# Kernel optimization log

Hardware: AMD Instinct MI355X
Metric: run time of the kernel (lower is better)

Reference implementation:

```python
import jax, jax.numpy as jnp
import numpy as np

T, B, D = 512, 32, 1280

def setup_inputs() -> dict:
    key = jax.random.key(0)
    k1, k2, k3, k4 = jax.random.split(key, 4)
    # W_h ~ orthogonal*0.9 in the original; a small-scale gaussian keeps the
    # recurrence spectral radius < 1 so tanh stays in its active range.
    return {
        "x_seq": jax.random.normal(k1, (T, B, D), dtype=jnp.float32),
        "z_seq": jax.random.normal(k2, (T, B, D), dtype=jnp.float32),
        "h0": jnp.zeros((B, D), dtype=jnp.float32),
        "W_x": jax.random.normal(k3, (D, D), dtype=jnp.float32) * (1.0 / np.sqrt(D)),
        "W_h": jax.random.normal(k4, (D, D), dtype=jnp.float32) * (0.9 / np.sqrt(D)),
        "b": jnp.zeros((D,), dtype=jnp.float32),
    }

def reference(x_seq, z_seq, h0, W_x, W_h, b):
    # Gated Elman scan (Mamba-style output gate):
    #   h_t = tanh(W_x x_t + W_h h_{t-1} + b)
    #   y_t = h_t * silu(z_t)
    # Hoist the input projection into one big GEMM: [T,B,D] x [D,D]^T.
    x_proj = jnp.einsum('tbd,ed->tbe', x_seq, W_x) + b  # [T,B,D]
    Wh_T = W_h.T  # [D,D], h @ Wh_T == Linear(h)

    def step(h, inp):
        xp, z = inp
        h_new = jnp.tanh(xp + h @ Wh_T)          # [B,D]
        y = h_new * jax.nn.silu(z)               # gated output
        return h_new, y

    h_last, output = jax.lax.scan(step, h0, (x_proj, z_seq))
    return output, h_last
```

## Files before the change

### kernel.cpp

```cpp
#include <hip/hip_runtime.h>
#include <math.h>

#define TT 512
#define BB 32
#define DD 1280

__launch_bounds__(256) __global__
void xproj_gemm(const float* __restrict__ X, const float* __restrict__ Wx,
                const float* __restrict__ bias, float* __restrict__ XP)
{
    __shared__ __align__(16) float As[16][64];
    __shared__ __align__(16) float Bs[16][64];
    const int tid = threadIdx.x;
    const int n0 = blockIdx.x * 64;
    const int m0 = blockIdx.y * 64;
    const int lm = tid >> 2;
    const int lk = (tid & 3) << 2;
    const int tn = tid & 15;
    const int tm = tid >> 4;

    float acc[4][4] = {};
    for (int k0 = 0; k0 < DD; k0 += 16) {
        float4 av = *(const float4*)(X  + (size_t)(m0 + lm) * DD + k0 + lk);
        float4 bv = *(const float4*)(Wx + (size_t)(n0 + lm) * DD + k0 + lk);
        __syncthreads();
        As[lk + 0][lm] = av.x; As[lk + 1][lm] = av.y;
        As[lk + 2][lm] = av.z; As[lk + 3][lm] = av.w;
        Bs[lk + 0][lm] = bv.x; Bs[lk + 1][lm] = bv.y;
        Bs[lk + 2][lm] = bv.z; Bs[lk + 3][lm] = bv.w;
        __syncthreads();
#pragma unroll
        for (int k = 0; k < 16; ++k) {
            float4 a4 = *(const float4*)&As[k][tm << 2];
            float4 b4 = *(const float4*)&Bs[k][tn << 2];
            float a[4] = {a4.x, a4.y, a4.z, a4.w};
            float b[4] = {b4.x, b4.y, b4.z, b4.w};
#pragma unroll
            for (int i = 0; i < 4; ++i)
#pragma unroll
                for (int j = 0; j < 4; ++j)
                    acc[i][j] += a[i] * b[j];
        }
    }
    float4 bv = *(const float4*)(bias + n0 + (tn << 2));
    float bias4[4] = {bv.x, bv.y, bv.z, bv.w};
#pragma unroll
    for (int i = 0; i < 4; ++i) {
        float4 o;
        o.x = acc[i][0] + bias4[0];
        o.y = acc[i][1] + bias4[1];
        o.z = acc[i][2] + bias4[2];
        o.w = acc[i][3] + bias4[3];
        *(float4*)(XP + (size_t)(m0 + (tm << 2) + i) * DD + n0 + (tn << 2)) = o;
    }
}

__device__ __forceinline__ unsigned long long ld_agent_u64(const unsigned long long* p) {
    return __hip_atomic_load(p, __ATOMIC_RELAXED, __HIP_MEMORY_SCOPE_AGENT);
}
__device__ __forceinline__ void st_agent_u64(unsigned long long* p, unsigned long long v) {
    __hip_atomic_store(p, v, __ATOMIC_RELAXED, __HIP_MEMORY_SCOPE_AGENT);
}

__global__ void init_ring(unsigned long long* __restrict__ ht)
{
    size_t i = (size_t)blockIdx.x * 256 + threadIdx.x;
    if (i < 2 * (size_t)BB * DD)
        st_agent_u64(ht + i, 0xFFFFFFFF00000000ull);
}

__launch_bounds__(256, 1) __global__
void gated_scan(const float* __restrict__ XP, const float* __restrict__ Z,
                const float* __restrict__ H0, const float* __restrict__ Wh,
                float* __restrict__ OUT,
                unsigned long long* __restrict__ ht)
{
    const int w   = blockIdx.x;
    const int g   = w & 7;
    const int idx = w >> 3;
    const int b0  = g << 2;
    const int e0  = idx * 40;
    const int tid = threadIdx.x;
    const int u   = tid >> 5;
    const int p   = tid & 31;

    __shared__ __align__(16) float S[2 * 4 * DD];

    const int d0 = p << 2;
    float4 wreg[5][10];
#pragma unroll 1
    for (int c = 0; c < 8; ++c) {
        __syncthreads();
        const float* src = Wh + (size_t)(e0 + 5 * c) * DD;
        for (int i = tid; i < 5 * DD / 4; i += 256)
            ((float4*)S)[i] = ((const float4*)src)[i];
        __syncthreads();
        if (u == c) {
#pragma unroll
            for (int j = 0; j < 5; ++j)
#pragma unroll
                for (int k = 0; k < 10; ++k)
                    wreg[j][k] = *(const float4*)&S[j * DD + d0 + (k << 7)];
        }
    }
    __syncthreads();

    const int  lo3 = p & 7;
    const bool fin = (lo3 != 3) && (lo3 < 6);
    const int  jj  = (lo3 < 3) ? lo3 : (lo3 - 1);
    const int  ii  = ((p >> 3) & 1) + (((p >> 4) & 1) << 1);
    const int  bb  = b0 + ii;
    const int  ee  = e0 + u * 5 + jj;

    unsigned long long v[20];

    for (int t = 1; t <= TT; ++t) {
        const size_t oidx = ((size_t)(t - 1) * BB + bb) * DD + ee;
        float xpv = 0.f, zv = 0.f;
        if (fin) { xpv = XP[oidx]; zv = Z[oidx]; }

        float* Sh = S + (size_t)(t & 1) * (4 * DD);
        if (t == 1) {
            const float* h0b = H0 + (size_t)b0 * DD;
#pragma unroll
            for (int i = 0; i < 20; ++i)
                Sh[i * 256 + tid] = h0b[i * 256 + tid];
        } else {
#pragma unroll
            for (int i = 0; i < 20; ++i)
                Sh[i * 256 + tid] = __uint_as_float((unsigned)v[i]);
        }
        __syncthreads();

        const unsigned long long* hn_ =
            ht + (size_t)(t & 1) * (BB * DD) + (size_t)b0 * DD;
        if (t < TT) {
#pragma unroll
            for (int i = 0; i < 20; ++i)
                v[i] = ld_agent_u64(hn_ + i * 256 + tid);
        }

        float acc[4][5] = {};
#pragma unroll
        for (int k = 0; k < 10; ++k) {
            const int d = d0 + (k << 7);
            float4 h4[4];
#pragma unroll
            for (int i = 0; i < 4; ++i)
                h4[i] = *(const float4*)&Sh[i * DD + d];
#pragma unroll
            for (int i = 0; i < 4; ++i)
#pragma unroll
                for (int j = 0; j < 5; ++j)
                    acc[i][j] += h4[i].x * wreg[j][k].x + h4[i].y * wreg[j][k].y
                               + h4[i].z * wreg[j][k].z + h4[i].w * wreg[j][k].w;
        }

        float s[20];
#pragma unroll
        for (int i = 0; i < 4; ++i)
#pragma unroll
            for (int j = 0; j < 5; ++j)
                s[i * 5 + j] = acc[i][j];
#pragma unroll
        for (int i = 0; i < 10; ++i) {
            float send = (p & 16) ? s[i] : s[10 + i];
            float recv = __shfl_xor(send, 16, 64);
            s[i] = ((p & 16) ? s[10 + i] : s[i]) + recv;
        }
#pragma unroll
        for (int i = 0; i < 5; ++i) {
            float send = (p & 8) ? s[i] : s[5 + i];
            float recv = __shfl_xor(send, 8, 64);
            s[i] = ((p & 8) ? s[5 + i] : s[i]) + recv;
        }
        s[5] = 0.f;
#pragma unroll
        for (int i = 0; i < 3; ++i) {
            float send = (p & 4) ? s[i] : s[3 + i];
            float recv = __shfl_xor(send, 4, 64);
            s[i] = ((p & 4) ? s[3 + i] : s[i]) + recv;
        }
        s[3] = 0.f;
#pragma unroll
        for (int i = 0; i < 2; ++i) {
            float send = (p & 2) ? s[i] : s[2 + i];
            float recv = __shfl_xor(send, 2, 64);
            s[i] = ((p & 2) ? s[2 + i] : s[i]) + recv;
        }
        {
            float send = (p & 1) ? s[0] : s[1];
            float recv = __shfl_xor(send, 1, 64);
            s[0] = ((p & 1) ? s[1] : s[0]) + recv;
        }

        if (fin) {
            const float hn = tanhf(xpv + s[0]);
            st_agent_u64(ht + (size_t)(t & 1) * (BB * DD) + (size_t)bb * DD + ee,
                         ((unsigned long long)(unsigned)t << 32) |
                         (unsigned long long)__float_as_uint(hn));
            const float sg = zv / (1.0f + __expf(-zv));
            OUT[oidx] = hn * sg;
            if (t == TT)
                OUT[(size_t)TT * BB * DD + (size_t)bb * DD + ee] = hn;
        }

        if (t < TT) {
            const unsigned need = (unsigned)t;
            bool bad;
            do {
                bad = false;
#pragma unroll
                for (int i = 0; i < 20; ++i)
                    if ((unsigned)(v[i] >> 32) != need) {
                        v[i] = ld_agent_u64(hn_ + i * 256 + tid);
                        bad = true;
                    }
            } while (bad);
        }
    }
}

extern "C" void kernel_launch(void* const* d_in, const int* in_sizes, int n_in,
                              void* d_out, int out_size, void* d_ws, size_t ws_size,
                              hipStream_t stream) {
    const float* x    = (const float*)d_in[0];
    const float* z    = (const float*)d_in[1];
    const float* h0   = (const float*)d_in[2];
    const float* Wx   = (const float*)d_in[3];
    const float* Wh   = (const float*)d_in[4];
    const float* bias = (const float*)d_in[5];
    float* out = (float*)d_out;

    float* xp = (float*)d_ws;
    unsigned long long* ht = (unsigned long long*)(xp + (size_t)TT * BB * DD);

    init_ring<<<(2 * BB * DD + 255) / 256, 256, 0, stream>>>(ht);

    dim3 ggrid(DD / 64, (TT * BB) / 64);
    xproj_gemm<<<ggrid, 256, 0, stream>>>(x, Wx, bias, xp);
    gated_scan<<<256, 256, 0, stream>>>(xp, z, h0, Wh, out, ht);
}
```

Before: 3.435 ms.

## Fuse input projection into persistent scan, overlapping it with the spin-wait

Removes the separate x-projection GEMM kernel and its workspace round trip. Each persistent block now keeps a slice of W_x in registers next to its W_h slice, stages the next timestep's x rows in shared memory, and computes the next x-projection while it waits for the other blocks' hidden state. This trades the GEMM launch and the XP traffic for doubled register pressure (two 200-float4 weight sets) and more work on the per-step critical path.

```diff
diff --git a/kernel.cpp b/kernel.cpp
--- a/kernel.cpp
+++ b/kernel.cpp
@@ -4,56 +4,6 @@
 #define TT 512
 #define BB 32
 #define DD 1280
-
-__launch_bounds__(256) __global__
-void xproj_gemm(const float* __restrict__ X, const float* __restrict__ Wx,
-                const float* __restrict__ bias, float* __restrict__ XP)
-{
-    __shared__ __align__(16) float As[16][64];
-    __shared__ __align__(16) float Bs[16][64];
-    const int tid = threadIdx.x;
-    const int n0 = blockIdx.x * 64;
-    const int m0 = blockIdx.y * 64;
-    const int lm = tid >> 2;
-    const int lk = (tid & 3) << 2;
-    const int tn = tid & 15;
-    const int tm = tid >> 4;
-
-    float acc[4][4] = {};
-    for (int k0 = 0; k0 < DD; k0 += 16) {
-        float4 av = *(const float4*)(X  + (size_t)(m0 + lm) * DD + k0 + lk);
-        float4 bv = *(const float4*)(Wx + (size_t)(n0 + lm) * DD + k0 + lk);
-        __syncthreads();
-        As[lk + 0][lm] = av.x; As[lk + 1][lm] = av.y;
-        As[lk + 2][lm] = av.z; As[lk + 3][lm] = av.w;
-        Bs[lk + 0][lm] = bv.x; Bs[lk + 1][lm] = bv.y;
-        Bs[lk + 2][lm] = bv.z; Bs[lk + 3][lm] = bv.w;
-        __syncthreads();
-#pragma unroll
-        for (int k = 0; k < 16; ++k) {
-            float4 a4 = *(const float4*)&As[k][tm << 2];
-            float4 b4 = *(const float4*)&Bs[k][tn << 2];
-            float a[4] = {a4.x, a4.y, a4.z, a4.w};
-            float b[4] = {b4.x, b4.y, b4.z, b4.w};
-#pragma unroll
-            for (int i = 0; i < 4; ++i)
-#pragma unroll
-                for (int j = 0; j < 4; ++j)
-                    acc[i][j] += a[i] * b[j];
-        }
-    }
-    float4 bv = *(const float4*)(bias + n0 + (tn << 2));
-    float bias4[4] = {bv.x, bv.y, bv.z, bv.w};
-#pragma unroll
-    for (int i = 0; i < 4; ++i) {
-        float4 o;
-        o.x = acc[i][0] + bias4[0];
-        o.y = acc[i][1] + bias4[1];
-        o.z = acc[i][2] + bias4[2];
-        o.w = acc[i][3] + bias4[3];
-        *(float4*)(XP + (size_t)(m0 + (tm << 2) + i) * DD + n0 + (tn << 2)) = o;
-    }
-}
 
 __device__ __forceinline__ unsigned long long ld_agent_u64(const unsigned long long* p) {
     return __hip_atomic_load(p, __ATOMIC_RELAXED, __HIP_MEMORY_SCOPE_AGENT);
@@ -69,11 +19,70 @@
         st_agent_u64(ht + i, 0xFFFFFFFF00000000ull);
 }
 
+__device__ __forceinline__ float dot_reduce(const float* __restrict__ Sbuf,
+                                            const float4 (&wr)[5][10],
+                                            int d0, int p)
+{
+    float acc[4][5] = {};
+#pragma unroll
+    for (int k = 0; k < 10; ++k) {
+        const int d = d0 + (k << 7);
+        float4 a4[4];
+#pragma unroll
+        for (int i = 0; i < 4; ++i)
+            a4[i] = *(const float4*)&Sbuf[i * DD + d];
+#pragma unroll
+        for (int i = 0; i < 4; ++i)
+#pragma unroll
+            for (int j = 0; j < 5; ++j)
+                acc[i][j] += a4[i].x * wr[j][k].x + a4[i].y * wr[j][k].y
+                           + a4[i].z * wr[j][k].z + a4[i].w * wr[j][k].w;
+    }
+    float s[20];
+#pragma unroll
+    for (int i = 0; i < 4; ++i)
+#pragma unroll
+        for (int j = 0; j < 5; ++j)
+            s[i * 5 + j] = acc[i][j];
+#pragma unroll
+    for (int i = 0; i < 10; ++i) {
+        float send = (p & 16) ? s[i] : s[10 + i];
+        float recv = __shfl_xor(send, 16, 64);
+        s[i] = ((p & 16) ? s[10 + i] : s[i]) + recv;
+    }
+#pragma unroll
+    for (int i = 0; i < 5; ++i) {
+        float send = (p & 8) ? s[i] : s[5 + i];
+        float recv = __shfl_xor(send, 8, 64);
+        s[i] = ((p & 8) ? s[5 + i] : s[i]) + recv;
+    }
+    s[5] = 0.f;
+#pragma unroll
+    for (int i = 0; i < 3; ++i) {
+        float send = (p & 4) ? s[i] : s[3 + i];
+        float recv = __shfl_xor(send, 4, 64);
+        s[i] = ((p & 4) ? s[3 + i] : s[i]) + recv;
+    }
+    s[3] = 0.f;
+#pragma unroll
+    for (int i = 0; i < 2; ++i) {
+        float send = (p & 2) ? s[i] : s[2 + i];
+        float recv = __shfl_xor(send, 2, 64);
+        s[i] = ((p & 2) ? s[2 + i] : s[i]) + recv;
+    }
+    {
+        float send = (p & 1) ? s[0] : s[1];
+        float recv = __shfl_xor(send, 1, 64);
+        s[0] = ((p & 1) ? s[1] : s[0]) + recv;
+    }
+    return s[0];
+}
+
 __launch_bounds__(256, 1) __global__
-void gated_scan(const float* __restrict__ XP, const float* __restrict__ Z,
-                const float* __restrict__ H0, const float* __restrict__ Wh,
-                float* __restrict__ OUT,
-                unsigned long long* __restrict__ ht)
+void fused_scan(const float* __restrict__ X, const float* __restrict__ Z,
+                const float* __restrict__ H0, const float* __restrict__ Wx,
+                const float* __restrict__ Wh, const float* __restrict__ bias,
+                float* __restrict__ OUT, unsigned long long* __restrict__ ht)
 {
     const int w   = blockIdx.x;
     const int g   = w & 7;
@@ -84,10 +93,12 @@
     const int u   = tid >> 5;
     const int p   = tid & 31;
 
-    __shared__ __align__(16) float S[2 * 4 * DD];
+    __shared__ __align__(16) float S [2 * 4 * DD];
+    __shared__ __align__(16) float Xs[2 * 4 * DD];
 
     const int d0 = p << 2;
     float4 wreg[5][10];
+    float4 wxreg[5][10];
 #pragma unroll 1
     for (int c = 0; c < 8; ++c) {
         __syncthreads();
@@ -101,6 +112,21 @@
 #pragma unroll
                 for (int k = 0; k < 10; ++k)
                     wreg[j][k] = *(const float4*)&S[j * DD + d0 + (k << 7)];
+        }
+    }
+#pragma unroll 1
+    for (int c = 0; c < 8; ++c) {
+        __syncthreads();
+        const float* src = Wx + (size_t)(e0 + 5 * c) * DD;
+        for (int i = tid; i < 5 * DD / 4; i += 256)
+            ((float4*)S)[i] = ((const float4*)src)[i];
+        __syncthreads();
+        if (u == c) {
+#pragma unroll
+            for (int j = 0; j < 5; ++j)
+#pragma unroll
+                for (int k = 0; k < 10; ++k)
+                    wxreg[j][k] = *(const float4*)&S[j * DD + d0 + (k << 7)];
         }
     }
     __syncthreads();
@@ -111,13 +137,23 @@
     const int  ii  = ((p >> 3) & 1) + (((p >> 4) & 1) << 1);
     const int  bb  = b0 + ii;
     const int  ee  = e0 + u * 5 + jj;
+    const float bias_lane = bias[ee];
+
+    {
+        const float* xg = X + (size_t)b0 * DD;
+#pragma unroll
+        for (int i = 0; i < 20; ++i)
+            Xs[i * 256 + tid] = xg[i * 256 + tid];
+    }
+    __syncthreads();
+    float xpv_cur = dot_reduce(Xs, wxreg, d0, p) + bias_lane;
 
     unsigned long long v[20];
 
     for (int t = 1; t <= TT; ++t) {
         const size_t oidx = ((size_t)(t - 1) * BB + bb) * DD + ee;
-        float xpv = 0.f, zv = 0.f;
-        if (fin) { xpv = XP[oidx]; zv = Z[oidx]; }
+        float zv = 0.f;
+        if (fin) zv = Z[oidx];
 
         float* Sh = S + (size_t)(t & 1) * (4 * DD);
         if (t == 1) {
@@ -130,7 +166,22 @@
             for (int i = 0; i < 20; ++i)
                 Sh[i * 256 + tid] = __uint_as_float((unsigned)v[i]);
         }
-        __syncthreads();
+        float* Xb = Xs + (size_t)(t & 1) * (4 * DD);
+        if (t < TT) {
+            const float* xg = X + ((size_t)t * BB + b0) * DD;
+#pragma unroll
+            for (int i = 0; i < 20; ++i)
+                Xb[i * 256 + tid] = xg[i * 256 + tid];
+        }
+        __syncthreads();
+
+        const float s0 = dot_reduce(Sh, wreg, d0, p);
+        const float hn = tanhf(xpv_cur + s0);
+
+        if (fin)
+            st_agent_u64(ht + (size_t)(t & 1) * (BB * DD) + (size_t)bb * DD + ee,
+                         ((unsigned long long)(unsigned)t << 32) |
+                         (unsigned long long)__float_as_uint(hn));
 
         const unsigned long long* hn_ =
             ht + (size_t)(t & 1) * (BB * DD) + (size_t)b0 * DD;
@@ -140,65 +191,7 @@
                 v[i] = ld_agent_u64(hn_ + i * 256 + tid);
         }
 
-        float acc[4][5] = {};
-#pragma unroll
-        for (int k = 0; k < 10; ++k) {
-            const int d = d0 + (k << 7);
-            float4 h4[4];
-#pragma unroll
-            for (int i = 0; i < 4; ++i)
-                h4[i] = *(const float4*)&Sh[i * DD + d];
-#pragma unroll
-            for (int i = 0; i < 4; ++i)
-#pragma unroll
-                for (int j = 0; j < 5; ++j)
-                    acc[i][j] += h4[i].x * wreg[j][k].x + h4[i].y * wreg[j][k].y
-                               + h4[i].z * wreg[j][k].z + h4[i].w * wreg[j][k].w;
-        }
-
-        float s[20];
-#pragma unroll
-        for (int i = 0; i < 4; ++i)
-#pragma unroll
-            for (int j = 0; j < 5; ++j)
-                s[i * 5 + j] = acc[i][j];
-#pragma unroll
-        for (int i = 0; i < 10; ++i) {
-            float send = (p & 16) ? s[i] : s[10 + i];
-            float recv = __shfl_xor(send, 16, 64);
-            s[i] = ((p & 16) ? s[10 + i] : s[i]) + recv;
-        }
-#pragma unroll
-        for (int i = 0; i < 5; ++i) {
-            float send = (p & 8) ? s[i] : s[5 + i];
-            float recv = __shfl_xor(send, 8, 64);
-            s[i] = ((p & 8) ? s[5 + i] : s[i]) + recv;
-        }
-        s[5] = 0.f;
-#pragma unroll
-        for (int i = 0; i < 3; ++i) {
-            float send = (p & 4) ? s[i] : s[3 + i];
-            float recv = __shfl_xor(send, 4, 64);
-            s[i] = ((p & 4) ? s[3 + i] : s[i]) + recv;
-        }
-        s[3] = 0.f;
-#pragma unroll
-        for (int i = 0; i < 2; ++i) {
-            float send = (p & 2) ? s[i] : s[2 + i];
-            float recv = __shfl_xor(send, 2, 64);
-            s[i] = ((p & 2) ? s[2 + i] : s[i]) + recv;
-        }
-        {
-            float send = (p & 1) ? s[0] : s[1];
-            float recv = __shfl_xor(send, 1, 64);
-            s[0] = ((p & 1) ? s[1] : s[0]) + recv;
-        }
-
         if (fin) {
-            const float hn = tanhf(xpv + s[0]);
-            st_agent_u64(ht + (size_t)(t & 1) * (BB * DD) + (size_t)bb * DD + ee,
-                         ((unsigned long long)(unsigned)t << 32) |
-                         (unsigned long long)__float_as_uint(hn));
             const float sg = zv / (1.0f + __expf(-zv));
             OUT[oidx] = hn * sg;
             if (t == TT)
@@ -206,6 +199,8 @@
         }
 
         if (t < TT) {
+            xpv_cur = dot_reduce(Xb, wxreg, d0, p) + bias_lane;
+
             const unsigned need = (unsigned)t;
             bool bad;
             do {
@@ -232,12 +227,8 @@
     const float* bias = (const float*)d_in[5];
     float* out = (float*)d_out;
 
-    float* xp = (float*)d_ws;
-    unsigned long long* ht = (unsigned long long*)(xp + (size_t)TT * BB * DD);
+    unsigned long long* ht = (unsigned long long*)d_ws;
 
     init_ring<<<(2 * BB * DD + 255) / 256, 256, 0, stream>>>(ht);
-
-    dim3 ggrid(DD / 64, (TT * BB) / 64);
-    xproj_gemm<<<ggrid, 256, 0, stream>>>(x, Wx, bias, xp);
-    gated_scan<<<256, 256, 0, stream>>>(xp, z, h0, Wh, out, ht);
-}
+    fused_scan<<<256, 256, 0, stream>>>(x, z, h0, Wx, Wh, bias, out, ht);
+}
```

Result: slower. 7.473 ms (+117.5%).
